# Kernel tuning notes

Hardware: AMD Instinct MI355X
Metric: run time of the kernel (lower is better)

Reference implementation:

```python
import jax, jax.numpy as jnp
import numpy as np

N = 50000      # nodes
E = 800000     # edges (before self-loops)
F = 128        # num_features
H = 64         # hidden_channels
B = 512        # batch_size (num graphs)
NC = 10        # num_classes


def setup_inputs() -> dict:
    key = jax.random.key(0)
    ks = jax.random.split(key, 24)
    rn = lambda k, shp, s=0.05: jax.random.normal(k, shp, jnp.float32) * s
    inp = {}
    inp["x"] = jax.random.normal(ks[0], (N, F), jnp.float32)
    inp["edge_index"] = jax.random.randint(ks[1], (2, E), 0, N)
    inp["batch"] = jnp.sort(jax.random.randint(ks[2], (N,), 0, B))
    # GATConv1: in F -> 4 heads x H (concat)
    inp["W1"] = rn(ks[3], (F, 4 * H)); inp["a_src1"] = rn(ks[4], (4, H))
    inp["a_dst1"] = rn(ks[5], (4, H)); inp["b1"] = rn(ks[6], (4 * H,))
    # GATConv2: in 4H -> 1 head x 2H
    inp["W2"] = rn(ks[7], (4 * H, 2 * H)); inp["a_src2"] = rn(ks[8], (1, 2 * H))
    inp["a_dst2"] = rn(ks[9], (1, 2 * H)); inp["b2"] = rn(ks[10], (2 * H,))
    # GCNConv: in 2H -> H
    inp["Wg"] = rn(ks[11], (2 * H, H)); inp["bg"] = rn(ks[12], (H,))
    # BatchNorms (eval mode: running_mean=0, running_var=1)
    inp["bn1_g"] = 1.0 + rn(ks[13], (4 * H,)); inp["bn1_b"] = rn(ks[14], (4 * H,))
    inp["bn2_g"] = 1.0 + rn(ks[15], (2 * H,)); inp["bn2_b"] = rn(ks[16], (2 * H,))
    inp["bn3_g"] = 1.0 + rn(ks[17], (2 * H,)); inp["bn3_b"] = rn(ks[18], (2 * H,))
    inp["lin1_W"] = rn(ks[19], (H, 128)); inp["lin1_b"] = rn(ks[20], (128,))
    inp["lin2_W"] = rn(ks[21], (128, NC)); inp["lin2_b"] = rn(ks[22], (NC,))
    inp["batch_size"] = B
    return inp


def _gat(x, src, dst, W, a_s, a_d, b, n):
    """PyG GATConv (eval): project, edge attention (leaky_relu 0.2), dst-softmax, scatter."""
    heads, ch = a_s.shape
    h = (x @ W).reshape(n, heads, ch)                       # [N, heads, ch]
    sc_s = (h * a_s).sum(-1)                                # [N, heads]
    sc_d = (h * a_d).sum(-1)
    e = jax.nn.leaky_relu(sc_s[src] + sc_d[dst], 0.2)       # [E2, heads]
    m = jax.ops.segment_max(e, dst, num_segments=n)
    ee = jnp.exp(e - m[dst])
    s = jax.ops.segment_sum(ee, dst, num_segments=n)
    alpha = ee / (s[dst] + 1e-16)                           # edge softmax per dst
    out = jax.ops.segment_sum(h[src] * alpha[:, :, None], dst, num_segments=n)
    return out.reshape(n, heads * ch) + b


def _bn_eval(x, g, b, eps=1e-5):
    # BatchNorm1d eval with running_mean=0, running_var=1
    return x * (g / jnp.sqrt(1.0 + eps)) + b


def reference(x, edge_index, batch, W1, a_src1, a_dst1, b1, W2, a_src2, a_dst2, b2,
              Wg, bg, bn1_g, bn1_b, bn2_g, bn2_b, bn3_g, bn3_b,
              lin1_W, lin1_b, lin2_W, lin2_b, batch_size):
    n = x.shape[0]
    loop = jnp.arange(n)
    src = jnp.concatenate([edge_index[0], loop])            # add self-loops (PyG default)
    dst = jnp.concatenate([edge_index[1], loop])
    lrelu = lambda v: jax.nn.leaky_relu(v, 0.01)            # module's LeakyReLU()

    x1 = _bn_eval(lrelu(_gat(x, src, dst, W1, a_src1, a_dst1, b1, n)), bn1_g, bn1_b)
    x2 = _bn_eval(lrelu(_gat(x1, src, dst, W2, a_src2, a_dst2, b2, n)), bn2_g, bn2_b)

    # GCNConv with symmetric normalization over A + I
    deg = jax.ops.segment_sum(jnp.ones_like(dst, jnp.float32), dst, num_segments=n)
    dis = jnp.where(deg > 0, jax.lax.rsqrt(deg), 0.0)
    h = x2 @ Wg                                             # [N, H]
    msg = h[src] * (dis[src] * dis[dst])[:, None]
    x3 = lrelu(jax.ops.segment_sum(msg, dst, num_segments=n) + bg)

    # global_mean_pool over graphs (dropout is identity in eval)
    sums = jax.ops.segment_sum(x3, batch, num_segments=batch_size)
    cnt = jax.ops.segment_sum(jnp.ones((n,), jnp.float32), batch, num_segments=batch_size)
    pooled = sums / jnp.clip(cnt, 1.0)[:, None]             # [B, H]

    y = lrelu(_bn_eval(pooled @ lin1_W + lin1_b, bn3_g, bn3_b))
    return y @ lin2_W + lin2_b                              # [B, NC]
```

## Files before the change

kernel.cpp:

```cpp
#include <hip/hip_runtime.h>
#include <hip/hip_bf16.h>

#define NN  50000
#define EE  800000
#define NE2 850000
#define NB  512
#define NRT 3125
#define NSB 196

#define BN_RS 0.9999950000374997f

typedef __attribute__((ext_vector_type(8))) short short8;
typedef __attribute__((ext_vector_type(4))) float f32x4;

__device__ __forceinline__ float bf2f(__hip_bfloat16 v) { return __bfloat162float(v); }
__device__ __forceinline__ unsigned short f2b(float v) {
    __hip_bfloat16 b = __float2bfloat16(v);
    return *reinterpret_cast<unsigned short*>(&b);
}
__device__ __forceinline__ float u2f(unsigned short u) {
    union { unsigned u; float f; } c; c.u = ((unsigned)u) << 16; return c.f;
}
__device__ __forceinline__ float4 u42f4(ushort4 v) {
    float4 r; r.x = u2f(v.x); r.y = u2f(v.y); r.z = u2f(v.z); r.w = u2f(v.w); return r;
}
__device__ __forceinline__ float lrelu01(float v) { return v > 0.f ? v : 0.01f * v; }
__device__ __forceinline__ float lrelu02(float v) { return v > 0.f ? v : 0.2f * v; }

__device__ __forceinline__ void edge_sd(const int* __restrict__ ei, int e, int& s, int& d) {
    if (e < EE) { s = ei[e]; d = ei[EE + e]; }
    else        { s = e - EE; d = e - EE; }
}

__device__ __forceinline__ float ldf(const void* p, int i, bool bf) {
    return bf ? bf2f(((const __hip_bfloat16*)p)[i]) : ((const float*)p)[i];
}

__global__ __launch_bounds__(256) void det_k(const unsigned* __restrict__ xw, int* __restrict__ flag) {
    __shared__ int cnt;
    if (threadIdx.x == 0) cnt = 0;
    __syncthreads();
    int c = 0;
#pragma unroll
    for (int k = 0; k < 4; ++k) {
        unsigned w = xw[threadIdx.x * 4 + k];
        unsigned ef = (w >> 7) & 0xFFu;
        if (ef >= 100u && ef <= 140u) c++;
    }
    atomicAdd(&cnt, c);
    __syncthreads();
    if (threadIdx.x == 0) *flag = (cnt > 512) ? 1 : 0;
}

__global__ __launch_bounds__(256) void conv_x_k(const void* __restrict__ x,
                                                ushort4* __restrict__ xb4,
                                                const int* __restrict__ flag) {
    bool bf = (*flag != 0);
    size_t i = (size_t)blockIdx.x * 256 + threadIdx.x;
    if (i >= (size_t)NN * 32) return;
    ushort4 o;
    if (bf) {
        o = ((const ushort4*)x)[i];
    } else {
        float4 v = ((const float4*)x)[i];
        o.x = f2b(v.x); o.y = f2b(v.y); o.z = f2b(v.z); o.w = f2b(v.w);
    }
    xb4[i] = o;
}

#define NSEG 20
#define WTOT 85578
#define PREP_TOT (WTOT + 32768 + 32768 + 8192)
struct SegArgs { const void* src[NSEG]; int off[NSEG]; };

__global__ __launch_bounds__(256) void prep_w_k(SegArgs a,
                                                const void* __restrict__ W1r,
                                                const void* __restrict__ W2r,
                                                const void* __restrict__ Wgr,
                                                float* __restrict__ wf,
                                                unsigned short* __restrict__ W1t,
                                                unsigned short* __restrict__ W2t,
                                                unsigned short* __restrict__ Wgt,
                                                const int* __restrict__ flag) {
    bool bf = (*flag != 0);
    int i = blockIdx.x * 256 + threadIdx.x;
    if (i >= PREP_TOT) return;
    if (i < WTOT) {
        int s = 0;
#pragma unroll
        for (int k = 1; k < NSEG; ++k) if (i >= a.off[k]) s = k;
        wf[i] = ldf(a.src[s], i - a.off[s], bf);
        return;
    }
    i -= WTOT;
    if (i < 32768) {
        int n = i >> 7, k = i & 127;
        W1t[i] = f2b(ldf(W1r, k * 256 + n, bf));
        return;
    }
    i -= 32768;
    if (i < 32768) {
        int n = i >> 8, k = i & 255;
        W2t[i] = f2b(ldf(W2r, k * 128 + n, bf));
        return;
    }
    i -= 32768;
    {
        int n = i >> 7, k = i & 127;
        Wgt[i] = f2b(ldf(Wgr, k * 64 + n, bf));
    }
}

__global__ __launch_bounds__(256) void deg_k(const int* __restrict__ ei, int* __restrict__ degi) {
    int e = blockIdx.x * 256 + threadIdx.x;
    if (e >= NE2) return;
    int s, d; edge_sd(ei, e, s, d);
    atomicAdd(&degi[d], 1);
}

__global__ __launch_bounds__(256) void pscan_k(const int* __restrict__ degi,
                                               int* __restrict__ incl, int* __restrict__ bsum) {
    __shared__ int tmp[256];
    int t = threadIdx.x;
    int i = blockIdx.x * 256 + t;
    int v = (i < NN) ? degi[i] : 0;
    tmp[t] = v;
    __syncthreads();
#pragma unroll
    for (int off = 1; off < 256; off <<= 1) {
        int u = (t >= off) ? tmp[t - off] : 0;
        __syncthreads();
        tmp[t] += u;
        __syncthreads();
    }
    if (i < NN) incl[i] = tmp[t];
    if (t == 255) bsum[blockIdx.x] = tmp[255];
}

__global__ __launch_bounds__(256) void bscan_k(int* __restrict__ bsum) {
    __shared__ int tmp[256];
    int t = threadIdx.x;
    tmp[t] = (t < NSB) ? bsum[t] : 0;
    __syncthreads();
#pragma unroll
    for (int off = 1; off < 256; off <<= 1) {
        int u = (t >= off) ? tmp[t - off] : 0;
        __syncthreads();
        tmp[t] += u;
        __syncthreads();
    }
    if (t < NSB) bsum[t] = tmp[t];
}

__global__ __launch_bounds__(256) void fscan_k(const int* __restrict__ degi,
                                               const int* __restrict__ incl,
                                               const int* __restrict__ bsum,
                                               int* __restrict__ row_ptr, int* __restrict__ cursor,
                                               float* __restrict__ dis) {
    int i = blockIdx.x * 256 + threadIdx.x;
    if (i >= NN) return;
    int dg = degi[i];
    int base = (blockIdx.x > 0) ? bsum[blockIdx.x - 1] : 0;
    int ex = base + incl[i] - dg;
    row_ptr[i] = ex; cursor[i] = ex;
    dis[i] = dg > 0 ? rsqrtf((float)dg) : 0.f;
    if (i == NN - 1) row_ptr[NN] = bsum[NSB - 1];
}

__global__ __launch_bounds__(256) void scatter_k(const int* __restrict__ ei,
                                                 int* __restrict__ cursor,
                                                 int* __restrict__ csr_src) {
    int e = blockIdx.x * 256 + threadIdx.x;
    if (e >= NE2) return;
    int s, d; edge_sd(ei, e, s, d);
    int pos = atomicAdd(&cursor[d], 1);
    csr_src[pos] = s;
}

template <int K, int NCOLS>
__global__ __launch_bounds__(256) void mgemm_k(const short* __restrict__ A,
                                               const short* __restrict__ Bt,
                                               unsigned short* __restrict__ C) {
    constexpr int CG = NCOLS / 64;
    int wave = threadIdx.x >> 6, lane = threadIdx.x & 63;
    int gidx = blockIdx.x * 4 + wave;
    if (gidx >= NRT * CG) return;
    int rt = gidx / CG, cg = gidx - rt * CG;
    int l15 = lane & 15, quad = lane >> 4;
    const short* ap = A + (size_t)(rt * 16 + l15) * K + quad * 8;
    const short* bp = Bt + (size_t)(cg * 64 + l15) * K + quad * 8;
    f32x4 acc[4] = {};
    for (int k0 = 0; k0 < K; k0 += 32) {
        short8 a = *(const short8*)(ap + k0);
#pragma unroll
        for (int j = 0; j < 4; ++j) {
            short8 b = *(const short8*)(bp + (size_t)j * 16 * K + k0);
            acc[j] = __builtin_amdgcn_mfma_f32_16x16x32_bf16(a, b, acc[j], 0, 0, 0);
        }
    }
#pragma unroll
    for (int j = 0; j < 4; ++j) {
        int n = cg * 64 + j * 16 + l15;
#pragma unroll
        for (int r = 0; r < 4; ++r) {
            int row = rt * 16 + quad * 4 + r;
            C[(size_t)row * NCOLS + n] = f2b(acc[j][r]);
        }
    }
}

__global__ __launch_bounds__(256) void scores1_k(const ushort4* __restrict__ h1b,
                                                 const float4* __restrict__ a_s4,
                                                 const float4* __restrict__ a_d4,
                                                 float* __restrict__ sc_s, float* __restrict__ sc_d) {
    int n = (blockIdx.x * 256 + threadIdx.x) >> 6;
    int lane = threadIdx.x & 63;
    if (n >= NN) return;
    float4 hv = u42f4(h1b[(size_t)n * 64 + lane]);
    float4 as = a_s4[lane], ad = a_d4[lane];
    float ps = hv.x * as.x + hv.y * as.y + hv.z * as.z + hv.w * as.w;
    float pd = hv.x * ad.x + hv.y * ad.y + hv.z * ad.z + hv.w * ad.w;
#pragma unroll
    for (int off = 1; off < 16; off <<= 1) { ps += __shfl_xor(ps, off); pd += __shfl_xor(pd, off); }
    if ((lane & 15) == 0) {
        int h = lane >> 4;
        sc_s[n * 4 + h] = ps; sc_d[n * 4 + h] = pd;
    }
}

__global__ __launch_bounds__(256) void scores2_k(const ushort2* __restrict__ h2b,
                                                 const float2* __restrict__ a_s2,
                                                 const float2* __restrict__ a_d2,
                                                 float* __restrict__ sc_s, float* __restrict__ sc_d) {
    int n = (blockIdx.x * 256 + threadIdx.x) >> 6;
    int lane = threadIdx.x & 63;
    if (n >= NN) return;
    ushort2 hu = h2b[(size_t)n * 64 + lane];
    float2 as = a_s2[lane], ad = a_d2[lane];
    float h0 = u2f(hu.x), h1 = u2f(hu.y);
    float ps = h0 * as.x + h1 * as.y;
    float pd = h0 * ad.x + h1 * ad.y;
#pragma unroll
    for (int off = 32; off; off >>= 1) { ps += __shfl_down(ps, off); pd += __shfl_down(pd, off); }
    if (lane == 0) { sc_s[n] = ps; sc_d[n] = pd; }
}

__device__ __forceinline__ float sel4(float4 v, int head) {
    float ab = (head & 1) ? v.y : v.x;
    float cd = (head & 1) ? v.w : v.z;
    return (head & 2) ? cd : ab;
}

__global__ __launch_bounds__(256) void agg1_k(const int* __restrict__ row_ptr,
                                              const int* __restrict__ csr_src,
                                              const ushort4* __restrict__ h1b,
                                              const float4* __restrict__ sc_s4,
                                              const float4* __restrict__ sc_d4,
                                              const float4* __restrict__ b1,
                                              const float4* __restrict__ g1,
                                              const float4* __restrict__ bb1,
                                              ushort4* __restrict__ x1b) {
    int n = (blockIdx.x * 256 + threadIdx.x) >> 6;
    int lane = threadIdx.x & 63;
    if (n >= NN) return;
    int row = row_ptr[n], end = row_ptr[n + 1];
    int head = lane >> 4;
    float scd_h = sel4(sc_d4[n], head);
    float4 acc = {0.f, 0.f, 0.f, 0.f};
    float den = 0.f;
    int c = row;
    for (; c + 3 < end; c += 4) {
        int s0 = csr_src[c], s1 = csr_src[c + 1], s2 = csr_src[c + 2], s3 = csr_src[c + 3];
        float4 scs0 = sc_s4[s0], scs1 = sc_s4[s1], scs2 = sc_s4[s2], scs3 = sc_s4[s3];
        float4 hv0 = u42f4(h1b[(size_t)s0 * 64 + lane]);
        float4 hv1 = u42f4(h1b[(size_t)s1 * 64 + lane]);
        float4 hv2 = u42f4(h1b[(size_t)s2 * 64 + lane]);
        float4 hv3 = u42f4(h1b[(size_t)s3 * 64 + lane]);
        float e0 = __expf(lrelu02(sel4(scs0, head) + scd_h));
        float e1 = __expf(lrelu02(sel4(scs1, head) + scd_h));
        float e2 = __expf(lrelu02(sel4(scs2, head) + scd_h));
        float e3 = __expf(lrelu02(sel4(scs3, head) + scd_h));
        den += (e0 + e1) + (e2 + e3);
        acc.x = fmaf(hv0.x, e0, fmaf(hv1.x, e1, fmaf(hv2.x, e2, fmaf(hv3.x, e3, acc.x))));
        acc.y = fmaf(hv0.y, e0, fmaf(hv1.y, e1, fmaf(hv2.y, e2, fmaf(hv3.y, e3, acc.y))));
        acc.z = fmaf(hv0.z, e0, fmaf(hv1.z, e1, fmaf(hv2.z, e2, fmaf(hv3.z, e3, acc.z))));
        acc.w = fmaf(hv0.w, e0, fmaf(hv1.w, e1, fmaf(hv2.w, e2, fmaf(hv3.w, e3, acc.w))));
    }
    for (; c < end; ++c) {
        int s0 = csr_src[c];
        float4 scs0 = sc_s4[s0];
        float4 hv0 = u42f4(h1b[(size_t)s0 * 64 + lane]);
        float e0 = __expf(lrelu02(sel4(scs0, head) + scd_h));
        den += e0;
        acc.x = fmaf(hv0.x, e0, acc.x);
        acc.y = fmaf(hv0.y, e0, acc.y);
        acc.z = fmaf(hv0.z, e0, acc.z);
        acc.w = fmaf(hv0.w, e0, acc.w);
    }
    float inv = 1.f / (den + 1e-16f);
    float4 bb = b1[lane], gg = g1[lane], be = bb1[lane];
    ushort4 o;
    o.x = f2b(lrelu01(acc.x * inv + bb.x) * (gg.x * BN_RS) + be.x);
    o.y = f2b(lrelu01(acc.y * inv + bb.y) * (gg.y * BN_RS) + be.y);
    o.z = f2b(lrelu01(acc.z * inv + bb.z) * (gg.z * BN_RS) + be.z);
    o.w = f2b(lrelu01(acc.w * inv + bb.w) * (gg.w * BN_RS) + be.w);
    x1b[(size_t)n * 64 + lane] = o;
}

__global__ __launch_bounds__(256) void agg2_k(const int* __restrict__ row_ptr,
                                              const int* __restrict__ csr_src,
                                              const ushort4* __restrict__ h2b,
                                              const float* __restrict__ sc_s,
                                              const float* __restrict__ sc_d,
                                              const float4* __restrict__ b2,
                                              const float4* __restrict__ g2,
                                              const float4* __restrict__ bb2,
                                              ushort4* __restrict__ x2b) {
    int n = (blockIdx.x * 256 + threadIdx.x) >> 6;
    int lane = threadIdx.x & 63;
    if (n >= NN) return;
    int g = lane >> 5, sl = lane & 31;
    int row = row_ptr[n], end = row_ptr[n + 1];
    float scd = sc_d[n];
    float4 acc = {0.f, 0.f, 0.f, 0.f};
    float den = 0.f;
    int c = row + g;
    for (; c + 2 < end; c += 4) {
        int s0 = csr_src[c], s1 = csr_src[c + 2];
        float sc0 = sc_s[s0], sc1 = sc_s[s1];
        float4 hv0 = u42f4(h2b[(size_t)s0 * 32 + sl]);
        float4 hv1 = u42f4(h2b[(size_t)s1 * 32 + sl]);
        float e0 = __expf(lrelu02(sc0 + scd));
        float e1 = __expf(lrelu02(sc1 + scd));
        den += e0 + e1;
        acc.x = fmaf(hv0.x, e0, fmaf(hv1.x, e1, acc.x));
        acc.y = fmaf(hv0.y, e0, fmaf(hv1.y, e1, acc.y));
        acc.z = fmaf(hv0.z, e0, fmaf(hv1.z, e1, acc.z));
        acc.w = fmaf(hv0.w, e0, fmaf(hv1.w, e1, acc.w));
    }
    if (c < end) {
        int s0 = csr_src[c];
        float e0 = __expf(lrelu02(sc_s[s0] + scd));
        float4 hv0 = u42f4(h2b[(size_t)s0 * 32 + sl]);
        den += e0;
        acc.x = fmaf(hv0.x, e0, acc.x);
        acc.y = fmaf(hv0.y, e0, acc.y);
        acc.z = fmaf(hv0.z, e0, acc.z);
        acc.w = fmaf(hv0.w, e0, acc.w);
    }
    den += __shfl_xor(den, 32);
    acc.x += __shfl_xor(acc.x, 32);
    acc.y += __shfl_xor(acc.y, 32);
    acc.z += __shfl_xor(acc.z, 32);
    acc.w += __shfl_xor(acc.w, 32);
    if (g == 0) {
        float inv = 1.f / (den + 1e-16f);
        float4 bb = b2[sl], gg = g2[sl], be = bb2[sl];
        ushort4 o;
        o.x = f2b(lrelu01(acc.x * inv + bb.x) * (gg.x * BN_RS) + be.x);
        o.y = f2b(lrelu01(acc.y * inv + bb.y) * (gg.y * BN_RS) + be.y);
        o.z = f2b(lrelu01(acc.z * inv + bb.z) * (gg.z * BN_RS) + be.z);
        o.w = f2b(lrelu01(acc.w * inv + bb.w) * (gg.w * BN_RS) + be.w);
        x2b[(size_t)n * 32 + sl] = o;
    }
}

__global__ __launch_bounds__(256) void gcn_k(const int* __restrict__ row_ptr,
                                             const int* __restrict__ csr_src,
                                             const ushort4* __restrict__ hgb,
                                             const float* __restrict__ dis,
                                             const float4* __restrict__ bg,
                                             float4* __restrict__ x3) {
    int n = (blockIdx.x * 256 + threadIdx.x) >> 6;
    int lane = threadIdx.x & 63;
    if (n >= NN) return;
    int g = lane >> 4, sl = lane & 15;
    int row = row_ptr[n], end = row_ptr[n + 1];
    float dn = dis[n];
    float4 acc = {0.f, 0.f, 0.f, 0.f};
    int c = row + g;
    for (; c + 4 < end; c += 8) {
        int s0 = csr_src[c], s1 = csr_src[c + 4];
        float w0 = dis[s0], w1 = dis[s1];
        float4 hv0 = u42f4(hgb[(size_t)s0 * 16 + sl]);
        float4 hv1 = u42f4(hgb[(size_t)s1 * 16 + sl]);
        acc.x = fmaf(hv0.x, w0, fmaf(hv1.x, w1, acc.x));
        acc.y = fmaf(hv0.y, w0, fmaf(hv1.y, w1, acc.y));
        acc.z = fmaf(hv0.z, w0, fmaf(hv1.z, w1, acc.z));
        acc.w = fmaf(hv0.w, w0, fmaf(hv1.w, w1, acc.w));
    }
    if (c < end) {
        int s0 = csr_src[c];
        float w0 = dis[s0];
        float4 hv0 = u42f4(hgb[(size_t)s0 * 16 + sl]);
        acc.x = fmaf(hv0.x, w0, acc.x);
        acc.y = fmaf(hv0.y, w0, acc.y);
        acc.z = fmaf(hv0.z, w0, acc.z);
        acc.w = fmaf(hv0.w, w0, acc.w);
    }
#pragma unroll
    for (int off = 16; off <= 32; off <<= 1) {
        acc.x += __shfl_xor(acc.x, off);
        acc.y += __shfl_xor(acc.y, off);
        acc.z += __shfl_xor(acc.z, off);
        acc.w += __shfl_xor(acc.w, off);
    }
    if (g == 0) {
        float4 bb = bg[sl];
        float4 o;
        o.x = lrelu01(acc.x * dn + bb.x);
        o.y = lrelu01(acc.y * dn + bb.y);
        o.z = lrelu01(acc.z * dn + bb.z);
        o.w = lrelu01(acc.w * dn + bb.w);
        x3[(size_t)n * 16 + sl] = o;
    }
}

__global__ __launch_bounds__(1024) void bounds_k(const int* __restrict__ batch, int* __restrict__ gstart) {
    int t = threadIdx.x;
    if (t > NB) return;
    int lo = 0, hi = NN;
    while (lo < hi) { int mid = (lo + hi) >> 1; if (batch[mid] < t) lo = mid + 1; else hi = mid; }
    gstart[t] = lo;
}

__global__ __launch_bounds__(256) void pool_k(const float* __restrict__ x3,
                                              const int* __restrict__ gstart,
                                              float* __restrict__ pooled) {
    __shared__ float red[4][64];
    int g = blockIdx.x, t = threadIdx.x;
    int c = t & 63, r = t >> 6;
    int s = gstart[g], e = gstart[g + 1];
    float sum = 0.f;
    for (int n = s + r; n < e; n += 4) sum += x3[(size_t)n * 64 + c];
    red[r][c] = sum;
    __syncthreads();
    if (t < 64) {
        float v = red[0][t] + red[1][t] + red[2][t] + red[3][t];
        int cnt = e - s; if (cnt < 1) cnt = 1;
        pooled[g * 64 + t] = v / (float)cnt;
    }
}

__global__ __launch_bounds__(128) void mlp_k(const float* __restrict__ pooled,
                                             const float* __restrict__ l1W,
                                             const float* __restrict__ l1b,
                                             const float* __restrict__ g3,
                                             const float* __restrict__ b3,
                                             const float* __restrict__ l2W,
                                             const float* __restrict__ l2b,
                                             void* __restrict__ outp,
                                             const int* __restrict__ flag) {
    __shared__ float pl[64];
    __shared__ float y1s[128];
    int g = blockIdx.x, t = threadIdx.x;
    if (t < 64) pl[t] = pooled[g * 64 + t];
    __syncthreads();
    float acc = l1b[t];
#pragma unroll 8
    for (int j = 0; j < 64; ++j) acc = fmaf(pl[j], l1W[j * 128 + t], acc);
    acc = acc * (g3[t] * BN_RS) + b3[t];
    y1s[t] = lrelu01(acc);
    __syncthreads();
    if (t < 10) {
        float o = l2b[t];
#pragma unroll 8
        for (int j = 0; j < 128; ++j) o = fmaf(y1s[j], l2W[j * 10 + t], o);
        if (*flag) ((__hip_bfloat16*)outp)[g * 10 + t] = __float2bfloat16(o);
        else       ((float*)outp)[g * 10 + t] = o;
    }
}

static const int kSegN[NSEG]  = {32768, 256, 256, 256, 32768, 128, 128, 128, 8192, 64,
                                 256, 256, 128, 128, 128, 128, 8192, 128, 1280, 10};
static const int kSegIn[NSEG] = {3, 4, 5, 6, 7, 8, 9, 10, 11, 12, 13, 14, 15, 16, 17, 18, 19, 20, 21, 22};

extern "C" void kernel_launch(void* const* d_in, const int* in_sizes, int n_in,
                              void* d_out, int out_size, void* d_ws, size_t ws_size,
                              hipStream_t stream) {
    const void* x_raw = d_in[0];
    const int*  ei    = (const int*)d_in[1];
    const int*  batch = (const int*)d_in[2];

    int*   flag = (int*)d_ws;
    float* ws   = (float*)d_ws;
    unsigned short* xb = (unsigned short*)(ws + 16);
    float* wf   = ws + 16 + (size_t)NN * 64;
    unsigned short* W1t = (unsigned short*)(wf + 85584);
    unsigned short* W2t = W1t + 32768;
    unsigned short* Wgt = W2t + 32768;
    unsigned short* h1b = Wgt + 8192;
    unsigned short* x1b = h1b + (size_t)NN * 256;
    unsigned short* x2b = x1b + (size_t)NN * 256;
    unsigned short* hgb = x2b + (size_t)NN * 128;
    float* x3   = (float*)(hgb + (size_t)NN * 64);
    float* sc_s1 = x3 + (size_t)NN * 64;
    float* sc_d1 = sc_s1 + (size_t)NN * 4;
    float* sc_s2 = sc_d1 + (size_t)NN * 4;
    float* sc_d2 = sc_s2 + NN;
    float* disb  = sc_d2 + NN;
    float* pooled = disb + NN;
    int*   gstart = (int*)(pooled + NB * 64);
    int*   degi   = gstart + NB + 4;
    int*   incl   = degi + NN;
    int*   bsum   = incl + NN;
    int*   row_ptr = bsum + 256;
    int*   cursor  = row_ptr + NN + 1;
    int*   csr_src = cursor + NN;

    int off[NSEG]; int o = 0;
    for (int s = 0; s < NSEG; ++s) { off[s] = o; o += kSegN[s]; }
    float* W1f  = wf + off[0];  float* as1f = wf + off[1];  float* ad1f = wf + off[2];
    float* b1f  = wf + off[3];  float* W2f  = wf + off[4];  float* as2f = wf + off[5];
    float* ad2f = wf + off[6];  float* b2f  = wf + off[7];  float* Wgf  = wf + off[8];
    float* bgf  = wf + off[9];  float* bn1g = wf + off[10]; float* bn1b = wf + off[11];
    float* bn2g = wf + off[12]; float* bn2b = wf + off[13]; float* bn3g = wf + off[14];
    float* bn3b = wf + off[15]; float* l1Wf = wf + off[16]; float* l1bf = wf + off[17];
    float* l2Wf = wf + off[18]; float* l2bf = wf + off[19];
    (void)W1f; (void)W2f; (void)Wgf;

    unsigned short* h2b = h1b;

    det_k<<<1, 256, 0, stream>>>((const unsigned*)x_raw, flag);
    conv_x_k<<<(NN * 32 + 255) / 256, 256, 0, stream>>>(x_raw, (ushort4*)xb, flag);
    SegArgs sa;
    for (int s = 0; s < NSEG; ++s) { sa.src[s] = d_in[kSegIn[s]]; sa.off[s] = off[s]; }
    prep_w_k<<<(PREP_TOT + 255) / 256, 256, 0, stream>>>(sa, d_in[3], d_in[7], d_in[11],
                                                         wf, W1t, W2t, Wgt, flag);

    hipMemsetAsync(degi, 0, NN * sizeof(int), stream);
    deg_k<<<(NE2 + 255) / 256, 256, 0, stream>>>(ei, degi);
    pscan_k<<<NSB, 256, 0, stream>>>(degi, incl, bsum);
    bscan_k<<<1, 256, 0, stream>>>(bsum);
    fscan_k<<<NSB, 256, 0, stream>>>(degi, incl, bsum, row_ptr, cursor, disb);
    scatter_k<<<(NE2 + 255) / 256, 256, 0, stream>>>(ei, cursor, csr_src);
    bounds_k<<<1, 1024, 0, stream>>>(batch, gstart);

    mgemm_k<128, 256><<<NRT, 256, 0, stream>>>((const short*)xb, (const short*)W1t, h1b);
    scores1_k<<<12500, 256, 0, stream>>>((const ushort4*)h1b, (const float4*)as1f,
                                         (const float4*)ad1f, sc_s1, sc_d1);
    agg1_k<<<12500, 256, 0, stream>>>(row_ptr, csr_src, (const ushort4*)h1b,
                                      (const float4*)sc_s1, (const float4*)sc_d1,
                                      (const float4*)b1f, (const float4*)bn1g,
                                      (const float4*)bn1b, (ushort4*)x1b);

    mgemm_k<256, 128><<<(NRT * 2 + 3) / 4, 256, 0, stream>>>((const short*)x1b, (const short*)W2t, h2b);
    scores2_k<<<12500, 256, 0, stream>>>((const ushort2*)h2b, (const float2*)as2f,
                                         (const float2*)ad2f, sc_s2, sc_d2);
    agg2_k<<<12500, 256, 0, stream>>>(row_ptr, csr_src, (const ushort4*)h2b,
                                      sc_s2, sc_d2,
                                      (const float4*)b2f, (const float4*)bn2g,
                                      (const float4*)bn2b, (ushort4*)x2b);

    mgemm_k<128, 64><<<(NRT + 3) / 4, 256, 0, stream>>>((const short*)x2b, (const short*)Wgt, hgb);
    gcn_k<<<12500, 256, 0, stream>>>(row_ptr, csr_src, (const ushort4*)hgb, disb,
                                     (const float4*)bgf, (float4*)x3);
    pool_k<<<NB, 256, 0, stream>>>(x3, gstart, pooled);

    mlp_k<<<NB, 128, 0, stream>>>(pooled, l1Wf, l1bf, bn3g, bn3b, l2Wf, l2bf, d_out, flag);
}
```

Baseline: 476.3 us.

## Fuse attention score computation into GEMM epilogues and merge x conversion into prep

Computes the GAT source/destination attention scores directly from the MFMA accumulators in the GEMM epilogue, so the separate scores1/scores2 kernels that re-read h1/h2 from memory are removed. The x-to-bf16 conversion is folded into the weight-prep kernel to save a launch. The aggregation kernels also mark the node index as wave-uniform via readfirstlane. Scores are now computed from fp32 accumulators rather than bf16-rounded values, which slightly changes numerics, and layer 2 needs an LDS cross-wave reduction plus a barrier.

```diff
diff --git a/kernel.cpp b/kernel.cpp
--- a/kernel.cpp
+++ b/kernel.cpp
@@ -52,39 +52,37 @@
     if (threadIdx.x == 0) *flag = (cnt > 512) ? 1 : 0;
 }
 
-__global__ __launch_bounds__(256) void conv_x_k(const void* __restrict__ x,
-                                                ushort4* __restrict__ xb4,
-                                                const int* __restrict__ flag) {
-    bool bf = (*flag != 0);
-    size_t i = (size_t)blockIdx.x * 256 + threadIdx.x;
-    if (i >= (size_t)NN * 32) return;
-    ushort4 o;
-    if (bf) {
-        o = ((const ushort4*)x)[i];
-    } else {
-        float4 v = ((const float4*)x)[i];
-        o.x = f2b(v.x); o.y = f2b(v.y); o.z = f2b(v.z); o.w = f2b(v.w);
-    }
-    xb4[i] = o;
-}
-
 #define NSEG 20
 #define WTOT 85578
-#define PREP_TOT (WTOT + 32768 + 32768 + 8192)
+#define XQUADS (NN * 32)
+#define PREP_TOT (XQUADS + WTOT + 32768 + 32768 + 8192)
 struct SegArgs { const void* src[NSEG]; int off[NSEG]; };
 
-__global__ __launch_bounds__(256) void prep_w_k(SegArgs a,
-                                                const void* __restrict__ W1r,
-                                                const void* __restrict__ W2r,
-                                                const void* __restrict__ Wgr,
-                                                float* __restrict__ wf,
-                                                unsigned short* __restrict__ W1t,
-                                                unsigned short* __restrict__ W2t,
-                                                unsigned short* __restrict__ Wgt,
-                                                const int* __restrict__ flag) {
+__global__ __launch_bounds__(256) void prep_k(SegArgs a,
+                                              const void* __restrict__ x_raw,
+                                              ushort4* __restrict__ xb4,
+                                              const void* __restrict__ W1r,
+                                              const void* __restrict__ W2r,
+                                              const void* __restrict__ Wgr,
+                                              float* __restrict__ wf,
+                                              unsigned short* __restrict__ W1t,
+                                              unsigned short* __restrict__ W2t,
+                                              unsigned short* __restrict__ Wgt,
+                                              const int* __restrict__ flag) {
     bool bf = (*flag != 0);
     int i = blockIdx.x * 256 + threadIdx.x;
     if (i >= PREP_TOT) return;
+    if (i < XQUADS) {
+        ushort4 o;
+        if (bf) o = ((const ushort4*)x_raw)[i];
+        else {
+            float4 v = ((const float4*)x_raw)[i];
+            o.x = f2b(v.x); o.y = f2b(v.y); o.z = f2b(v.z); o.w = f2b(v.w);
+        }
+        xb4[i] = o;
+        return;
+    }
+    i -= XQUADS;
     if (i < WTOT) {
         int s = 0;
 #pragma unroll
@@ -177,72 +175,159 @@
     csr_src[pos] = s;
 }
 
-template <int K, int NCOLS>
-__global__ __launch_bounds__(256) void mgemm_k(const short* __restrict__ A,
-                                               const short* __restrict__ Bt,
-                                               unsigned short* __restrict__ C) {
-    constexpr int CG = NCOLS / 64;
+__global__ __launch_bounds__(256) void mgemm1_k(const short* __restrict__ A,
+                                                const short* __restrict__ Bt,
+                                                unsigned short* __restrict__ C,
+                                                const float* __restrict__ a_s,
+                                                const float* __restrict__ a_d,
+                                                float* __restrict__ sc_s,
+                                                float* __restrict__ sc_d) {
+    int wave = threadIdx.x >> 6, lane = threadIdx.x & 63;
+    int rt = blockIdx.x, cg = wave;
+    int l15 = lane & 15, quad = lane >> 4;
+    const short* ap = A + (size_t)(rt * 16 + l15) * 128 + quad * 8;
+    const short* bp = Bt + (size_t)(cg * 64 + l15) * 128 + quad * 8;
+    f32x4 acc[4] = {};
+    for (int k0 = 0; k0 < 128; k0 += 32) {
+        short8 a = *(const short8*)(ap + k0);
+#pragma unroll
+        for (int j = 0; j < 4; ++j) {
+            short8 b = *(const short8*)(bp + (size_t)j * 16 * 128 + k0);
+            acc[j] = __builtin_amdgcn_mfma_f32_16x16x32_bf16(a, b, acc[j], 0, 0, 0);
+        }
+    }
+    float asv[4], adv[4];
+#pragma unroll
+    for (int j = 0; j < 4; ++j) {
+        asv[j] = a_s[cg * 64 + j * 16 + l15];
+        adv[j] = a_d[cg * 64 + j * 16 + l15];
+    }
+    float ss[4] = {0.f, 0.f, 0.f, 0.f}, sd[4] = {0.f, 0.f, 0.f, 0.f};
+#pragma unroll
+    for (int j = 0; j < 4; ++j) {
+        int n = cg * 64 + j * 16 + l15;
+#pragma unroll
+        for (int r = 0; r < 4; ++r) {
+            float v = acc[j][r];
+            C[(size_t)(rt * 16 + quad * 4 + r) * 256 + n] = f2b(v);
+            ss[r] = fmaf(v, asv[j], ss[r]);
+            sd[r] = fmaf(v, adv[j], sd[r]);
+        }
+    }
+#pragma unroll
+    for (int off = 1; off < 16; off <<= 1) {
+#pragma unroll
+        for (int r = 0; r < 4; ++r) {
+            ss[r] += __shfl_xor(ss[r], off);
+            sd[r] += __shfl_xor(sd[r], off);
+        }
+    }
+    if (l15 == 0) {
+#pragma unroll
+        for (int r = 0; r < 4; ++r) {
+            int node = rt * 16 + quad * 4 + r;
+            sc_s[node * 4 + cg] = ss[r];
+            sc_d[node * 4 + cg] = sd[r];
+        }
+    }
+}
+
+__global__ __launch_bounds__(256) void mgemm2_k(const short* __restrict__ A,
+                                                const short* __restrict__ Bt,
+                                                unsigned short* __restrict__ C,
+                                                const float* __restrict__ a_s,
+                                                const float* __restrict__ a_d,
+                                                float* __restrict__ sc_s,
+                                                float* __restrict__ sc_d) {
+    __shared__ float sred[4][16][2];
     int wave = threadIdx.x >> 6, lane = threadIdx.x & 63;
     int gidx = blockIdx.x * 4 + wave;
-    if (gidx >= NRT * CG) return;
-    int rt = gidx / CG, cg = gidx - rt * CG;
+    bool act = gidx < NRT * 2;
+    int gcl = act ? gidx : NRT * 2 - 1;
+    int rt = gcl >> 1, cg = gcl & 1;
     int l15 = lane & 15, quad = lane >> 4;
-    const short* ap = A + (size_t)(rt * 16 + l15) * K + quad * 8;
-    const short* bp = Bt + (size_t)(cg * 64 + l15) * K + quad * 8;
+    const short* ap = A + (size_t)(rt * 16 + l15) * 256 + quad * 8;
+    const short* bp = Bt + (size_t)(cg * 64 + l15) * 256 + quad * 8;
     f32x4 acc[4] = {};
-    for (int k0 = 0; k0 < K; k0 += 32) {
+    for (int k0 = 0; k0 < 256; k0 += 32) {
         short8 a = *(const short8*)(ap + k0);
 #pragma unroll
         for (int j = 0; j < 4; ++j) {
-            short8 b = *(const short8*)(bp + (size_t)j * 16 * K + k0);
+            short8 b = *(const short8*)(bp + (size_t)j * 16 * 256 + k0);
             acc[j] = __builtin_amdgcn_mfma_f32_16x16x32_bf16(a, b, acc[j], 0, 0, 0);
         }
     }
+    float asv[4], adv[4];
+#pragma unroll
+    for (int j = 0; j < 4; ++j) {
+        asv[j] = a_s[cg * 64 + j * 16 + l15];
+        adv[j] = a_d[cg * 64 + j * 16 + l15];
+    }
+    float ss[4] = {0.f, 0.f, 0.f, 0.f}, sd[4] = {0.f, 0.f, 0.f, 0.f};
 #pragma unroll
     for (int j = 0; j < 4; ++j) {
         int n = cg * 64 + j * 16 + l15;
 #pragma unroll
         for (int r = 0; r < 4; ++r) {
-            int row = rt * 16 + quad * 4 + r;
-            C[(size_t)row * NCOLS + n] = f2b(acc[j][r]);
-        }
-    }
-}
-
-__global__ __launch_bounds__(256) void scores1_k(const ushort4* __restrict__ h1b,
-                                                 const float4* __restrict__ a_s4,
-                                                 const float4* __restrict__ a_d4,
-                                                 float* __restrict__ sc_s, float* __restrict__ sc_d) {
-    int n = (blockIdx.x * 256 + threadIdx.x) >> 6;
-    int lane = threadIdx.x & 63;
-    if (n >= NN) return;
-    float4 hv = u42f4(h1b[(size_t)n * 64 + lane]);
-    float4 as = a_s4[lane], ad = a_d4[lane];
-    float ps = hv.x * as.x + hv.y * as.y + hv.z * as.z + hv.w * as.w;
-    float pd = hv.x * ad.x + hv.y * ad.y + hv.z * ad.z + hv.w * ad.w;
-#pragma unroll
-    for (int off = 1; off < 16; off <<= 1) { ps += __shfl_xor(ps, off); pd += __shfl_xor(pd, off); }
-    if ((lane & 15) == 0) {
-        int h = lane >> 4;
-        sc_s[n * 4 + h] = ps; sc_d[n * 4 + h] = pd;
-    }
-}
-
-__global__ __launch_bounds__(256) void scores2_k(const ushort2* __restrict__ h2b,
-                                                 const float2* __restrict__ a_s2,
-                                                 const float2* __restrict__ a_d2,
-                                                 float* __restrict__ sc_s, float* __restrict__ sc_d) {
-    int n = (blockIdx.x * 256 + threadIdx.x) >> 6;
-    int lane = threadIdx.x & 63;
-    if (n >= NN) return;
-    ushort2 hu = h2b[(size_t)n * 64 + lane];
-    float2 as = a_s2[lane], ad = a_d2[lane];
-    float h0 = u2f(hu.x), h1 = u2f(hu.y);
-    float ps = h0 * as.x + h1 * as.y;
-    float pd = h0 * ad.x + h1 * ad.y;
-#pragma unroll
-    for (int off = 32; off; off >>= 1) { ps += __shfl_down(ps, off); pd += __shfl_down(pd, off); }
-    if (lane == 0) { sc_s[n] = ps; sc_d[n] = pd; }
+            float v = acc[j][r];
+            if (act) C[(size_t)(rt * 16 + quad * 4 + r) * 128 + n] = f2b(v);
+            ss[r] = fmaf(v, asv[j], ss[r]);
+            sd[r] = fmaf(v, adv[j], sd[r]);
+        }
+    }
+#pragma unroll
+    for (int off = 1; off < 16; off <<= 1) {
+#pragma unroll
+        for (int r = 0; r < 4; ++r) {
+            ss[r] += __shfl_xor(ss[r], off);
+            sd[r] += __shfl_xor(sd[r], off);
+        }
+    }
+    if (l15 == 0) {
+#pragma unroll
+        for (int r = 0; r < 4; ++r) {
+            sred[wave][quad * 4 + r][0] = ss[r];
+            sred[wave][quad * 4 + r][1] = sd[r];
+        }
+    }
+    __syncthreads();
+    if (threadIdx.x < 32) {
+        int rl = threadIdx.x >> 4, row = threadIdx.x & 15;
+        int g2 = blockIdx.x * 4 + rl * 2;
+        if (g2 < NRT * 2) {
+            int node = (g2 >> 1) * 16 + row;
+            sc_s[node] = sred[rl * 2][row][0] + sred[rl * 2 + 1][row][0];
+            sc_d[node] = sred[rl * 2][row][1] + sred[rl * 2 + 1][row][1];
+        }
+    }
+}
+
+__global__ __launch_bounds__(256) void mgemm3_k(const short* __restrict__ A,
+                                                const short* __restrict__ Bt,
+                                                unsigned short* __restrict__ C) {
+    int wave = threadIdx.x >> 6, lane = threadIdx.x & 63;
+    int gidx = blockIdx.x * 4 + wave;
+    if (gidx >= NRT) return;
+    int rt = gidx;
+    int l15 = lane & 15, quad = lane >> 4;
+    const short* ap = A + (size_t)(rt * 16 + l15) * 128 + quad * 8;
+    const short* bp = Bt + (size_t)l15 * 128 + quad * 8;
+    f32x4 acc[4] = {};
+    for (int k0 = 0; k0 < 128; k0 += 32) {
+        short8 a = *(const short8*)(ap + k0);
+#pragma unroll
+        for (int j = 0; j < 4; ++j) {
+            short8 b = *(const short8*)(bp + (size_t)j * 16 * 128 + k0);
+            acc[j] = __builtin_amdgcn_mfma_f32_16x16x32_bf16(a, b, acc[j], 0, 0, 0);
+        }
+    }
+#pragma unroll
+    for (int j = 0; j < 4; ++j) {
+        int n = j * 16 + l15;
+#pragma unroll
+        for (int r = 0; r < 4; ++r)
+            C[(size_t)(rt * 16 + quad * 4 + r) * 64 + n] = f2b(acc[j][r]);
+    }
 }
 
 __device__ __forceinline__ float sel4(float4 v, int head) {
@@ -260,7 +345,7 @@
                                               const float4* __restrict__ g1,
                                               const float4* __restrict__ bb1,
                                               ushort4* __restrict__ x1b) {
-    int n = (blockIdx.x * 256 + threadIdx.x) >> 6;
+    int n = __builtin_amdgcn_readfirstlane((blockIdx.x * 256 + threadIdx.x) >> 6);
     int lane = threadIdx.x & 63;
     if (n >= NN) return;
     int row = row_ptr[n], end = row_ptr[n + 1];
@@ -316,7 +401,7 @@
                                               const float4* __restrict__ g2,
                                               const float4* __restrict__ bb2,
                                               ushort4* __restrict__ x2b) {
-    int n = (blockIdx.x * 256 + threadIdx.x) >> 6;
+    int n = __builtin_amdgcn_readfirstlane((blockIdx.x * 256 + threadIdx.x) >> 6);
     int lane = threadIdx.x & 63;
     if (n >= NN) return;
     int g = lane >> 5, sl = lane & 31;
@@ -371,7 +456,7 @@
                                              const float* __restrict__ dis,
                                              const float4* __restrict__ bg,
                                              float4* __restrict__ x3) {
-    int n = (blockIdx.x * 256 + threadIdx.x) >> 6;
+    int n = __builtin_amdgcn_readfirstlane((blockIdx.x * 256 + threadIdx.x) >> 6);
     int lane = threadIdx.x & 63;
     if (n >= NN) return;
     int g = lane >> 4, sl = lane & 15;
@@ -510,23 +595,22 @@
 
     int off[NSEG]; int o = 0;
     for (int s = 0; s < NSEG; ++s) { off[s] = o; o += kSegN[s]; }
-    float* W1f  = wf + off[0];  float* as1f = wf + off[1];  float* ad1f = wf + off[2];
-    float* b1f  = wf + off[3];  float* W2f  = wf + off[4];  float* as2f = wf + off[5];
-    float* ad2f = wf + off[6];  float* b2f  = wf + off[7];  float* Wgf  = wf + off[8];
+    float* as1f = wf + off[1];  float* ad1f = wf + off[2];
+    float* b1f  = wf + off[3];  float* as2f = wf + off[5];
+    float* ad2f = wf + off[6];  float* b2f  = wf + off[7];
     float* bgf  = wf + off[9];  float* bn1g = wf + off[10]; float* bn1b = wf + off[11];
     float* bn2g = wf + off[12]; float* bn2b = wf + off[13]; float* bn3g = wf + off[14];
     float* bn3b = wf + off[15]; float* l1Wf = wf + off[16]; float* l1bf = wf + off[17];
     float* l2Wf = wf + off[18]; float* l2bf = wf + off[19];
-    (void)W1f; (void)W2f; (void)Wgf;
 
     unsigned short* h2b = h1b;
 
     det_k<<<1, 256, 0, stream>>>((const unsigned*)x_raw, flag);
-    conv_x_k<<<(NN * 32 + 255) / 256, 256, 0, stream>>>(x_raw, (ushort4*)xb, flag);
     SegArgs sa;
     for (int s = 0; s < NSEG; ++s) { sa.src[s] = d_in[kSegIn[s]]; sa.off[s] = off[s]; }
-    prep_w_k<<<(PREP_TOT + 255) / 256, 256, 0, stream>>>(sa, d_in[3], d_in[7], d_in[11],
-                                                         wf, W1t, W2t, Wgt, flag);
+    prep_k<<<(PREP_TOT + 255) / 256, 256, 0, stream>>>(sa, x_raw, (ushort4*)xb,
+                                                       d_in[3], d_in[7], d_in[11],
+                                                       wf, W1t, W2t, Wgt, flag);
 
     hipMemsetAsync(degi, 0, NN * sizeof(int), stream);
     deg_k<<<(NE2 + 255) / 256, 256, 0, stream>>>(ei, degi);
@@ -536,23 +620,21 @@
     scatter_k<<<(NE2 + 255) / 256, 256, 0, stream>>>(ei, cursor, csr_src);
     bounds_k<<<1, 1024, 0, stream>>>(batch, gstart);
 
-    mgemm_k<128, 256><<<NRT, 256, 0, stream>>>((const short*)xb, (const short*)W1t, h1b);
-    scores1_k<<<12500, 256, 0, stream>>>((const ushort4*)h1b, (const float4*)as1f,
-                                         (const float4*)ad1f, sc_s1, sc_d1);
+    mgemm1_k<<<NRT, 256, 0, stream>>>((const short*)xb, (const short*)W1t, h1b,
+                                      as1f, ad1f, sc_s1, sc_d1);
     agg1_k<<<12500, 256, 0, stream>>>(row_ptr, csr_src, (const ushort4*)h1b,
                                       (const float4*)sc_s1, (const float4*)sc_d1,
                                       (const float4*)b1f, (const float4*)bn1g,
                                       (const float4*)bn1b, (ushort4*)x1b);
 
-    mgemm_k<256, 128><<<(NRT * 2 + 3) / 4, 256, 0, stream>>>((const short*)x1b, (const short*)W2t, h2b);
-    scores2_k<<<12500, 256, 0, stream>>>((const ushort2*)h2b, (const float2*)as2f,
-                                         (const float2*)ad2f, sc_s2, sc_d2);
+    mgemm2_k<<<(NRT * 2 + 3) / 4, 256, 0, stream>>>((const short*)x1b, (const short*)W2t, h2b,
+                                                    as2f, ad2f, sc_s2, sc_d2);
     agg2_k<<<12500, 256, 0, stream>>>(row_ptr, csr_src, (const ushort4*)h2b,
                                       sc_s2, sc_d2,
                                       (const float4*)b2f, (const float4*)bn2g,
                                       (const float4*)bn2b, (ushort4*)x2b);
 
-    mgemm_k<128, 64><<<(NRT + 3) / 4, 256, 0, stream>>>((const short*)x2b, (const short*)Wgt, hgb);
+    mgemm3_k<<<(NRT + 3) / 4, 256, 0, stream>>>((const short*)x2b, (const short*)Wgt, hgb);
     gcn_k<<<12500, 256, 0, stream>>>(row_ptr, csr_src, (const ushort4*)hgb, disb,
                                      (const float4*)bgf, (float4*)x3);
     pool_k<<<NB, 256, 0, stream>>>(x3, gstart, pooled);
```

Measured after the change: 458.9 us. 1.04x faster.
